# Performance work log

Hardware: AMD Instinct MI355X
Metric: run time of the kernel (lower is better)

## Reference

```python
import jax, jax.numpy as jnp
import numpy as np

N_HEADS = 32
N_KV_HEADS = 8
HEAD_DIM = 128
ROPE_BASE = 10000.0
NEG_INF = -1e9


def rope(x, base=ROPE_BASE, offset=0):
    # x: [B, H, L, d]; 'traditional' RoPE with the module's rotation formula.
    d = x.shape[-1]
    t = jnp.arange(x.shape[2], dtype=jnp.float32) + offset
    freqs = base ** (-jnp.arange(0, d, 2, dtype=jnp.float32) / d)  # [d/2]
    ang = t[:, None] * freqs[None, :]                              # [L, d/2]
    cos, sin = jnp.cos(ang), jnp.sin(ang)
    x1, x2 = x[..., 0::2], x[..., 1::2]
    out = jnp.stack([x1 * cos + x2 * sin, x1 * sin - x2 * cos], axis=-1)
    return out.reshape(x.shape)


def setup_inputs() -> dict:
    key = jax.random.key(0)
    ks = jax.random.split(key, 5)
    B, L, D = 2, 2048, 4096
    x = jax.random.normal(ks[0], (B, L, D), dtype=jnp.float32)
    wq = jax.random.normal(ks[1], (D, N_HEADS * HEAD_DIM), dtype=jnp.float32) * 0.02
    wk = jax.random.normal(ks[2], (D, N_KV_HEADS * HEAD_DIM), dtype=jnp.float32) * 0.02
    wv = jax.random.normal(ks[3], (D, N_KV_HEADS * HEAD_DIM), dtype=jnp.float32) * 0.02
    wo = jax.random.normal(ks[4], (N_HEADS * HEAD_DIM, D), dtype=jnp.float32) * 0.02
    # causal additive mask [L, L]
    mask = jnp.where(jnp.tril(jnp.ones((L, L), dtype=bool)), 0.0, NEG_INF).astype(jnp.float32)
    return {"x": x, "mask": mask, "wq": wq, "wk": wk, "wv": wv, "wo": wo}


def reference(x, mask, wq, wk, wv, wo):
    B, L, D = x.shape
    scale = HEAD_DIM ** -0.5
    q = (x @ wq).reshape(B, L, N_HEADS, HEAD_DIM).transpose(0, 2, 1, 3)     # [B,H,L,d]
    k = (x @ wk).reshape(B, L, N_KV_HEADS, HEAD_DIM).transpose(0, 2, 1, 3)  # [B,Hk,L,d]
    v = (x @ wv).reshape(B, L, N_KV_HEADS, HEAD_DIM).transpose(0, 2, 1, 3)
    rep = N_HEADS // N_KV_HEADS
    k = jnp.repeat(k, rep, axis=1)  # [B,H,L,d]  (physical GQA repeat, as in source)
    v = jnp.repeat(v, rep, axis=1)
    q = rope(q)
    k = rope(k)
    scores = jnp.einsum("bhqd,bhkd->bhqk", q * scale, k) + mask  # [B,H,L,L]
    probs = jax.nn.softmax(scores.astype(jnp.float32), axis=-1).astype(scores.dtype)
    out = jnp.einsum("bhqk,bhkd->bhqd", probs, v)
    out = out.transpose(0, 2, 1, 3).reshape(B, L, N_HEADS * HEAD_DIM)
    return out @ wo, (k, v)
```

## Files before the change

kernel.cpp:

```cpp
#include <hip/hip_runtime.h>

typedef unsigned short u16;
typedef unsigned int u32;
typedef float f32x4 __attribute__((ext_vector_type(4)));
typedef u32 u32x2 __attribute__((ext_vector_type(2)));
typedef __bf16 bf16x8 __attribute__((ext_vector_type(8)));

#define DEV __device__ __forceinline__

DEV u16 f2b(float f) {
    union { float f; u32 u; } v; v.f = f;
    u32 r = v.u + 0x7fffu + ((v.u >> 16) & 1u);
    return (u16)(r >> 16);
}
DEV float b2f(u16 b) {
    union { u32 u; float f; } v; v.u = ((u32)b) << 16;
    return v.f;
}

DEV void gload16(const void* g, void* l) {
    __builtin_amdgcn_global_load_lds((const __attribute__((address_space(1))) void*)g,
                                     (__attribute__((address_space(3))) void*)l, 16, 0, 0);
}

DEV f32x4 mfma16(bf16x8 a, bf16x8 b, f32x4 c) {
    return __builtin_amdgcn_mfma_f32_16x16x32_bf16(a, b, c, 0, 0, 0);
}

__global__ __launch_bounds__(256) void convx_kernel(const float* __restrict__ in,
                                                    u16* __restrict__ out) {
    size_t i = ((size_t)blockIdx.x * 256 + threadIdx.x) * 4;
    float4 v = *(const float4*)(in + i);
    ushort4 o; o.x = f2b(v.x); o.y = f2b(v.y); o.z = f2b(v.z); o.w = f2b(v.w);
    *(ushort4*)(out + i) = o;
}

__global__ __launch_bounds__(256) void tconv_kernel(const float* __restrict__ in,
                                                    u16* __restrict__ out, int K, int N) {
    __shared__ float tile[64][65];
    int t = threadIdx.x;
    int n0 = blockIdx.x * 64, k0 = blockIdx.y * 64;
    int r = t >> 4, c4 = (t & 15) * 4;
#pragma unroll
    for (int i = 0; i < 4; ++i) {
        float4 v = *(const float4*)(in + (size_t)(k0 + i * 16 + r) * N + n0 + c4);
        tile[i * 16 + r][c4 + 0] = v.x; tile[i * 16 + r][c4 + 1] = v.y;
        tile[i * 16 + r][c4 + 2] = v.z; tile[i * 16 + r][c4 + 3] = v.w;
    }
    __syncthreads();
#pragma unroll
    for (int i = 0; i < 4; ++i) {
        int nn = i * 16 + r;
        ushort4 o;
        o.x = f2b(tile[c4 + 0][nn]); o.y = f2b(tile[c4 + 1][nn]);
        o.z = f2b(tile[c4 + 2][nn]); o.w = f2b(tile[c4 + 3][nn]);
        *(ushort4*)(out + (size_t)(n0 + nn) * K + k0 + c4) = o;
    }
}

__global__ __launch_bounds__(512, 1) void gemm192_kernel(const u16* __restrict__ A,
                                                         const u16* __restrict__ Bt,
                                                         u16* __restrict__ Cb,
                                                         int N, int K, int gy) {
    __shared__ __align__(16) u16 Asb[2][2][128 * 64];
    __shared__ __align__(16) u16 Bsb[2][192 * 64];
    int t = threadIdx.x;
    int lane = t & 63, w = t >> 6;
    int wrM = w >> 2, wcN = w & 3;
    int lr = lane & 15, hi = lane >> 4;
    int wg = blockIdx.x;
    int swz = (wg & 7) * ((int)gridDim.x >> 3) + (wg >> 3);
    int bx = swz / gy, by = swz % gy;
    int m0 = by * 256, n0 = bx * 192;
    int nk = K >> 6;

    auto stageA = [&](int X) {
        const u16* src = A + (size_t)m0 * K + X * 64;
        char* dst = (char*)&Asb[X & 1][0][0];
#pragma unroll
        for (int it = 0; it < 4; ++it) {
            int c = it * 512 + t;
            int row = c >> 3;
            int col8 = ((c & 7) ^ (row & 7)) << 3;
            gload16(src + (size_t)row * K + col8, dst + (it * 512 + (t & ~63)) * 16);
        }
    };
    auto stageB = [&](int X) {
        const u16* src = Bt + (size_t)n0 * K + X * 64;
        char* dst = (char*)&Bsb[X & 1][0];
#pragma unroll
        for (int it = 0; it < 3; ++it) {
            int c = it * 512 + t;
            int row = c >> 3;
            int col8 = ((c & 7) ^ (row & 7)) << 3;
            gload16(src + (size_t)row * K + col8, dst + (it * 512 + (t & ~63)) * 16);
        }
    };

    stageA(0); stageB(0); stageA(1); stageB(1);
    asm volatile("s_waitcnt vmcnt(7)" ::: "memory");
    __builtin_amdgcn_s_barrier();

    f32x4 acc[8][3] = {};
    for (int kt = 0; kt < nk; ++kt) {
        __builtin_amdgcn_sched_barrier(0);
        int p = kt & 1;
        const char* Ah = (const char*)&Asb[p][wrM][0];
        const char* Bh = (const char*)&Bsb[p][0];
        bool s1 = (kt + 1 < nk), s2 = (kt + 2 < nk);
        bf16x8 a[8][2], bb[2][2], bc[2];

#pragma unroll
        for (int mf = 0; mf < 4; ++mf)
#pragma unroll
            for (int ks = 0; ks < 2; ++ks) {
                int row = mf * 16 + lr;
                a[mf][ks] = *(const bf16x8*)(Ah + ((row * 128 + ks * 64 + hi * 16) ^ ((row & 7) << 4)));
            }
#pragma unroll
        for (int nf = 0; nf < 2; ++nf)
#pragma unroll
            for (int ks = 0; ks < 2; ++ks) {
                int row = wcN * 48 + nf * 16 + lr;
                bb[nf][ks] = *(const bf16x8*)(Bh + ((row * 128 + ks * 64 + hi * 16) ^ ((row & 7) << 4)));
            }
        __builtin_amdgcn_s_barrier();
        __builtin_amdgcn_s_setprio(1);
#pragma unroll
        for (int mf = 0; mf < 4; ++mf)
#pragma unroll
            for (int nf = 0; nf < 2; ++nf)
#pragma unroll
                for (int ks = 0; ks < 2; ++ks)
                    acc[mf][nf] = mfma16(a[mf][ks], bb[nf][ks], acc[mf][nf]);
        __builtin_amdgcn_s_setprio(0);
        __builtin_amdgcn_s_barrier();

#pragma unroll
        for (int mf = 4; mf < 8; ++mf)
#pragma unroll
            for (int ks = 0; ks < 2; ++ks) {
                int row = mf * 16 + lr;
                a[mf][ks] = *(const bf16x8*)(Ah + ((row * 128 + ks * 64 + hi * 16) ^ ((row & 7) << 4)));
            }
        __builtin_amdgcn_s_barrier();
        __builtin_amdgcn_s_setprio(1);
#pragma unroll
        for (int mf = 4; mf < 8; ++mf)
#pragma unroll
            for (int nf = 0; nf < 2; ++nf)
#pragma unroll
                for (int ks = 0; ks < 2; ++ks)
                    acc[mf][nf] = mfma16(a[mf][ks], bb[nf][ks], acc[mf][nf]);
        __builtin_amdgcn_s_setprio(0);
        __builtin_amdgcn_s_barrier();

#pragma unroll
        for (int ks = 0; ks < 2; ++ks) {
            int row = wcN * 48 + 32 + lr;
            bc[ks] = *(const bf16x8*)(Bh + ((row * 128 + ks * 64 + hi * 16) ^ ((row & 7) << 4)));
        }
        if (s2) stageA(kt + 2);
        __builtin_amdgcn_s_barrier();
        __builtin_amdgcn_s_setprio(1);
#pragma unroll
        for (int mf = 4; mf < 8; ++mf)
#pragma unroll
            for (int ks = 0; ks < 2; ++ks)
                acc[mf][2] = mfma16(a[mf][ks], bc[ks], acc[mf][2]);
        __builtin_amdgcn_s_setprio(0);
        __builtin_amdgcn_s_barrier();

        if (s2) stageB(kt + 2);
        __builtin_amdgcn_s_barrier();
        __builtin_amdgcn_s_setprio(1);
#pragma unroll
        for (int mf = 0; mf < 4; ++mf)
#pragma unroll
            for (int ks = 0; ks < 2; ++ks)
                acc[mf][2] = mfma16(a[mf][ks], bc[ks], acc[mf][2]);
        __builtin_amdgcn_s_setprio(0);
        if (s1) {
            if (s2) asm volatile("s_waitcnt vmcnt(7)" ::: "memory");
            else    asm volatile("s_waitcnt vmcnt(0)" ::: "memory");
        }
        __builtin_amdgcn_s_barrier();
    }

#pragma unroll
    for (int mf = 0; mf < 8; ++mf)
#pragma unroll
        for (int nf = 0; nf < 3; ++nf)
#pragma unroll
            for (int r = 0; r < 4; ++r) {
                int m = m0 + wrM * 128 + mf * 16 + hi * 4 + r;
                int n = n0 + wcN * 48 + nf * 16 + lr;
                Cb[(size_t)m * N + n] = f2b(acc[mf][nf][r]);
            }
}

template <bool F32OUT>
__global__ __launch_bounds__(512, 1) void gemm256_kernel(const u16* __restrict__ A,
                                                         const u16* __restrict__ Bt,
                                                         u16* __restrict__ Cb,
                                                         float* __restrict__ Cf,
                                                         int M, int N, int K, int gy) {
    __shared__ __align__(16) u16 Asb[2][2][128 * 64];
    __shared__ __align__(16) u16 Bsb[2][2][128 * 64];
    (void)M;
    int t = threadIdx.x;
    int lane = t & 63, w = t >> 6;
    int wrM = w >> 2, wcN = w & 3;
    int lr = lane & 15, hi = lane >> 4;
    int wg = blockIdx.x;
    int swz = (wg & 7) * ((int)gridDim.x >> 3) + (wg >> 3);
    int bx = swz / gy, by = swz % gy;
    int m0 = by * 256, n0 = bx * 256;
    int nk = K >> 6;

    auto stageA = [&](int X, int h) {
        const u16* src = A + (size_t)(m0 + h * 128) * K + X * 64;
        char* dst = (char*)&Asb[X & 1][h][0];
#pragma unroll
        for (int it = 0; it < 2; ++it) {
            int c = it * 512 + t;
            int row = c >> 3;
            int col8 = ((c & 7) ^ (row & 7)) << 3;
            gload16(src + (size_t)row * K + col8, dst + (it * 512 + (t & ~63)) * 16);
        }
    };
    auto stageB = [&](int X, int h) {
        const u16* src = Bt + (size_t)(n0 + h * 128) * K + X * 64;
        char* dst = (char*)&Bsb[X & 1][h][0];
#pragma unroll
        for (int it = 0; it < 2; ++it) {
            int c = it * 512 + t;
            int row = c >> 3;
            int col8 = ((c & 7) ^ (row & 7)) << 3;
            gload16(src + (size_t)row * K + col8, dst + (it * 512 + (t & ~63)) * 16);
        }
    };

    stageA(0, 0); stageA(0, 1); stageB(0, 0); stageB(0, 1);
    stageA(1, 0); stageA(1, 1); stageB(1, 0);
    asm volatile("s_waitcnt vmcnt(6)" ::: "memory");
    __builtin_amdgcn_s_barrier();

    f32x4 acc[8][4] = {};
    for (int kt = 0; kt < nk; ++kt) {
        __builtin_amdgcn_sched_barrier(0);
        int p = kt & 1;
        const char* Ah = (const char*)&Asb[p][wrM][0];
        const char* Bh = (const char*)&Bsb[p][wcN >> 1][0];
        bool s1 = (kt + 1 < nk), s2 = (kt + 2 < nk);
        bf16x8 a[8][2], bb[2][2];

#pragma unroll
        for (int mf = 0; mf < 4; ++mf)
#pragma unroll
            for (int ks = 0; ks < 2; ++ks) {
                int row = mf * 16 + lr;
                a[mf][ks] = *(const bf16x8*)(Ah + ((row * 128 + ks * 64 + hi * 16) ^ ((row & 7) << 4)));
            }
#pragma unroll
        for (int nf = 0; nf < 2; ++nf)
#pragma unroll
            for (int ks = 0; ks < 2; ++ks) {
                int row = (wcN & 1) * 64 + nf * 16 + lr;
                bb[nf][ks] = *(const bf16x8*)(Bh + ((row * 128 + ks * 64 + hi * 16) ^ ((row & 7) << 4)));
            }
        if (s1) stageB(kt + 1, 1);
        __builtin_amdgcn_s_barrier();
        __builtin_amdgcn_s_setprio(1);
#pragma unroll
        for (int mf = 0; mf < 4; ++mf)
#pragma unroll
            for (int nf = 0; nf < 2; ++nf)
#pragma unroll
                for (int ks = 0; ks < 2; ++ks)
                    acc[mf][nf] = mfma16(a[mf][ks], bb[nf][ks], acc[mf][nf]);
        __builtin_amdgcn_s_setprio(0);
        __builtin_amdgcn_s_barrier();

#pragma unroll
        for (int mf = 4; mf < 8; ++mf)
#pragma unroll
            for (int ks = 0; ks < 2; ++ks) {
                int row = mf * 16 + lr;
                a[mf][ks] = *(const bf16x8*)(Ah + ((row * 128 + ks * 64 + hi * 16) ^ ((row & 7) << 4)));
            }
        __builtin_amdgcn_s_barrier();
        __builtin_amdgcn_s_setprio(1);
#pragma unroll
        for (int mf = 4; mf < 8; ++mf)
#pragma unroll
            for (int nf = 0; nf < 2; ++nf)
#pragma unroll
                for (int ks = 0; ks < 2; ++ks)
                    acc[mf][nf] = mfma16(a[mf][ks], bb[nf][ks], acc[mf][nf]);
        __builtin_amdgcn_s_setprio(0);
        __builtin_amdgcn_s_barrier();

#pragma unroll
        for (int nf = 0; nf < 2; ++nf)
#pragma unroll
            for (int ks = 0; ks < 2; ++ks) {
                int row = (wcN & 1) * 64 + (nf + 2) * 16 + lr;
                bb[nf][ks] = *(const bf16x8*)(Bh + ((row * 128 + ks * 64 + hi * 16) ^ ((row & 7) << 4)));
            }
        if (s2) { stageA(kt + 2, 0); stageA(kt + 2, 1); }
        __builtin_amdgcn_s_barrier();
        __builtin_amdgcn_s_setprio(1);
#pragma unroll
        for (int mf = 4; mf < 8; ++mf)
#pragma unroll
            for (int nf = 0; nf < 2; ++nf)
#pragma unroll
                for (int ks = 0; ks < 2; ++ks)
                    acc[mf][nf + 2] = mfma16(a[mf][ks], bb[nf][ks], acc[mf][nf + 2]);
        __builtin_amdgcn_s_setprio(0);
        __builtin_amdgcn_s_barrier();

        if (s2) stageB(kt + 2, 0);
        __builtin_amdgcn_s_barrier();
        __builtin_amdgcn_s_setprio(1);
#pragma unroll
        for (int mf = 0; mf < 4; ++mf)
#pragma unroll
            for (int nf = 0; nf < 2; ++nf)
#pragma unroll
                for (int ks = 0; ks < 2; ++ks)
                    acc[mf][nf + 2] = mfma16(a[mf][ks], bb[nf][ks], acc[mf][nf + 2]);
        __builtin_amdgcn_s_setprio(0);
        if (s1) {
            if (s2) asm volatile("s_waitcnt vmcnt(6)" ::: "memory");
            else    asm volatile("s_waitcnt vmcnt(0)" ::: "memory");
        }
        __builtin_amdgcn_s_barrier();
    }

#pragma unroll
    for (int mf = 0; mf < 8; ++mf)
#pragma unroll
        for (int nf = 0; nf < 4; ++nf)
#pragma unroll
            for (int r = 0; r < 4; ++r) {
                int m = m0 + wrM * 128 + mf * 16 + hi * 4 + r;
                int n = n0 + wcN * 64 + nf * 16 + lr;
                if (F32OUT) Cf[(size_t)m * N + n] = acc[mf][nf][r];
                else        Cb[(size_t)m * N + n] = f2b(acc[mf][nf][r]);
            }
}

__global__ __launch_bounds__(256) void rope_kernel(u16* __restrict__ qkv,
                                                   float* __restrict__ outk) {
    int row = blockIdx.y;
    int p = blockIdx.x * 256 + threadIdx.x;
    int b = row >> 11, l = row & 2047;
    float freq = exp2f((float)(p & 63) * -0.2076205059304601f);
    float sv, cv; sincosf((float)l * freq, &sv, &cv);
    if (p < 2048) {
        int h = p >> 6, i = p & 63;
        size_t idx = (size_t)row * 6144 + h * 128 + 2 * i;
        u32 pr = *(const u32*)(qkv + idx);
        float x1 = b2f((u16)(pr & 0xffff)), x2 = b2f((u16)(pr >> 16));
        float o1 = x1 * cv + x2 * sv, o2 = x1 * sv - x2 * cv;
        *(u32*)(qkv + idx) = (u32)f2b(o1) | ((u32)f2b(o2) << 16);
    } else {
        int kvh = (p >> 6) - 32, i = p & 63;
        size_t idx = (size_t)row * 6144 + 4096 + kvh * 128 + 2 * i;
        u32 pr = *(const u32*)(qkv + idx);
        float x1 = b2f((u16)(pr & 0xffff)), x2 = b2f((u16)(pr >> 16));
        float o1 = x1 * cv + x2 * sv, o2 = x1 * sv - x2 * cv;
        *(u32*)(qkv + idx) = (u32)f2b(o1) | ((u32)f2b(o2) << 16);
#pragma unroll
        for (int r = 0; r < 4; ++r) {
            float2 o; o.x = o1; o.y = o2;
            *(float2*)(outk + ((size_t)((b * 32 + kvh * 4 + r) * 2048) + l) * 128 + 2 * i) = o;
        }
    }
}

__global__ __launch_bounds__(256) void vtrans_kernel(const u16* __restrict__ qkv,
                                                     u16* __restrict__ vt,
                                                     float* __restrict__ outv) {
    __shared__ u16 tile[64][65];
    int t = threadIdx.x;
    int l0 = blockIdx.x * 64, d0 = blockIdx.y * 64;
    int z = blockIdx.z, b = z >> 3, kvh = z & 7;
    int r = t >> 4, c4 = (t & 15) * 4;
#pragma unroll
    for (int i = 0; i < 4; ++i) {
        int l = l0 + i * 16 + r;
        ushort4 v = *(const ushort4*)(qkv + (size_t)(b * 2048 + l) * 6144 + 5120 + kvh * 128 + d0 + c4);
        tile[i * 16 + r][c4 + 0] = v.x; tile[i * 16 + r][c4 + 1] = v.y;
        tile[i * 16 + r][c4 + 2] = v.z; tile[i * 16 + r][c4 + 3] = v.w;
        float4 f; f.x = b2f(v.x); f.y = b2f(v.y); f.z = b2f(v.z); f.w = b2f(v.w);
#pragma unroll
        for (int rr = 0; rr < 4; ++rr)
            *(float4*)(outv + ((size_t)((b * 32 + kvh * 4 + rr) * 2048) + l) * 128 + d0 + c4) = f;
    }
    __syncthreads();
#pragma unroll
    for (int i = 0; i < 4; ++i) {
        int dn = i * 16 + r;
        ushort4 o;
        o.x = tile[c4 + 0][dn]; o.y = tile[c4 + 1][dn];
        o.z = tile[c4 + 2][dn]; o.w = tile[c4 + 3][dn];
        *(ushort4*)(vt + (size_t)((b * 8 + kvh) * 128 + d0 + dn) * 2048 + l0 + c4) = o;
    }
}

__global__ __launch_bounds__(256) void attn_kernel(const u16* __restrict__ qkv,
                                                   const u16* __restrict__ vt,
                                                   u16* __restrict__ ab) {
    __shared__ __align__(16) u16 Kbuf[2][64 * 128];
    __shared__ __align__(16) u16 Vbuf[2][128 * 64];
    __shared__ __align__(16) u16 Ps[4][16 * 64];
    int t = threadIdx.x, lane = t & 63, w = t >> 6;
    int lr = lane & 15, hi = lane >> 4;
    int h = blockIdx.y, b = blockIdx.z, kvh = h >> 2;

    const u16* kbase = qkv + (size_t)(b * 2048) * 6144 + 4096 + kvh * 128;
    const u16* vtbase = vt + (size_t)((b * 8 + kvh) * 128) * 2048;

    auto stageKV = [&](int k0, int buf) {
#pragma unroll
        for (int i = 0; i < 4; ++i) {
            int c = i * 256 + t;
            int row = c >> 4;
            int col8 = ((c & 15) ^ (row & 7)) << 3;
            gload16(kbase + (size_t)(k0 + row) * 6144 + col8,
                    (char*)Kbuf[buf] + (i * 256 + (t & ~63)) * 16);
        }
#pragma unroll
        for (int i = 0; i < 4; ++i) {
            int c = i * 256 + t;
            int row = c >> 3;
            int col8 = ((c & 7) ^ (row & 7)) << 3;
            gload16(vtbase + (size_t)row * 2048 + k0 + col8,
                    (char*)Vbuf[buf] + (i * 256 + (t & ~63)) * 16);
        }
    };

    auto process = [&](int qblk) {
        int q0 = qblk * 64;
        int qr = w * 16 + lr;
        bf16x8 qf[4];
#pragma unroll
        for (int kki = 0; kki < 4; ++kki)
            qf[kki] = *(const bf16x8*)(qkv + (size_t)(b * 2048 + q0 + qr) * 6144 + h * 128 +
                                       kki * 32 + 8 * hi);
        f32x4 acc[8] = {};
        float mrun = -1e30f, lrun = 0.f;

        int nt = qblk + 1;
        stageKV(0, 0);
        __syncthreads();
        int cur = 0;
        for (int kt = 0; kt < nt; ++kt) {
            if (kt + 1 < nt) stageKV((kt + 1) * 64, cur ^ 1);
            __builtin_amdgcn_sched_barrier(0);

            const u16* Ks = Kbuf[cur];
            const u16* Vs = Vbuf[cur];
            f32x4 s[4] = {};
            __builtin_amdgcn_s_setprio(1);
#pragma unroll
            for (int kki = 0; kki < 4; ++kki) {
                bf16x8 kf[4];
#pragma unroll
                for (int fc = 0; fc < 4; ++fc) {
                    int kvr = fc * 16 + lr;
                    int byt = (kvr * 256 + (kki * 32 + 8 * hi) * 2) ^ ((kvr & 7) << 4);
                    kf[fc] = *(const bf16x8*)((const char*)Ks + byt);
                }
#pragma unroll
                for (int fc = 0; fc < 4; ++fc) s[fc] = mfma16(kf[fc], qf[kki], s[fc]);
            }
            __builtin_amdgcn_s_setprio(0);
            const float SC = 0.08838834764831845f;
            int diag = (kt == nt - 1);
#pragma unroll
            for (int fc = 0; fc < 4; ++fc)
#pragma unroll
                for (int r = 0; r < 4; ++r) {
                    float v = s[fc][r] * SC;
                    if (diag && (fc * 16 + hi * 4 + r) > qr) v = -1e30f;
                    s[fc][r] = v;
                }
            float pm = s[0][0];
#pragma unroll
            for (int fc = 0; fc < 4; ++fc)
#pragma unroll
                for (int r = 0; r < 4; ++r) pm = fmaxf(pm, s[fc][r]);
            pm = fmaxf(pm, __shfl_xor(pm, 16));
            pm = fmaxf(pm, __shfl_xor(pm, 32));
            float mn = fmaxf(mrun, pm);
            float fr = __expf(mrun - mn);
            mrun = mn;
            float ls = 0.f;
#pragma unroll
            for (int fc = 0; fc < 4; ++fc)
#pragma unroll
                for (int r = 0; r < 4; ++r) {
                    float e = __expf(s[fc][r] - mn);
                    s[fc][r] = e;
                    ls += e;
                }
            ls += __shfl_xor(ls, 16);
            ls += __shfl_xor(ls, 32);
            lrun = lrun * fr + ls;
#pragma unroll
            for (int dhf = 0; dhf < 8; ++dhf)
#pragma unroll
                for (int r = 0; r < 4; ++r) acc[dhf][r] *= fr;
            u16* Pw = Ps[w];
#pragma unroll
            for (int fc = 0; fc < 4; ++fc) {
                u32x2 pk;
                pk.x = (u32)f2b(s[fc][0]) | ((u32)f2b(s[fc][1]) << 16);
                pk.y = (u32)f2b(s[fc][2]) | ((u32)f2b(s[fc][3]) << 16);
                int byt = (lr * 128 + fc * 32 + hi * 8) ^ ((lr & 7) << 4);
                *(u32x2*)((char*)Pw + byt) = pk;
            }
            asm volatile("s_waitcnt lgkmcnt(0)" ::: "memory");
            __builtin_amdgcn_s_setprio(1);
#pragma unroll
            for (int kk2 = 0; kk2 < 2; ++kk2) {
                int bytp = (lr * 128 + kk2 * 64 + hi * 16) ^ ((lr & 7) << 4);
                bf16x8 pf = *(const bf16x8*)((const char*)Pw + bytp);
#pragma unroll
                for (int dhf = 0; dhf < 8; ++dhf) {
                    int dh = dhf * 16 + lr;
                    int bytv = (dh * 128 + (kk2 * 32 + 8 * hi) * 2) ^ ((dh & 7) << 4);
                    bf16x8 vf = *(const bf16x8*)((const char*)Vs + bytv);
                    acc[dhf] = mfma16(vf, pf, acc[dhf]);
                }
            }
            __builtin_amdgcn_s_setprio(0);
            __syncthreads();
            cur ^= 1;
        }
        float inv = 1.0f / lrun;
        int qrow = q0 + qr;
#pragma unroll
        for (int dhf = 0; dhf < 8; ++dhf) {
            ushort4 o;
            o.x = f2b(acc[dhf][0] * inv); o.y = f2b(acc[dhf][1] * inv);
            o.z = f2b(acc[dhf][2] * inv); o.w = f2b(acc[dhf][3] * inv);
            *(ushort4*)(ab + (size_t)(b * 2048 + qrow) * 4096 + h * 128 + dhf * 16 + hi * 4) = o;
        }
    };

    process(31 - blockIdx.x);
    __syncthreads();
    process(blockIdx.x);
}

extern "C" void kernel_launch(void* const* d_in, const int* in_sizes, int n_in,
                              void* d_out, int out_size, void* d_ws, size_t ws_size,
                              hipStream_t stream) {
    (void)in_sizes; (void)n_in; (void)out_size; (void)ws_size;
    const float* x  = (const float*)d_in[0];
    const float* wq = (const float*)d_in[2];
    const float* wk = (const float*)d_in[3];
    const float* wv = (const float*)d_in[4];
    const float* wo = (const float*)d_in[5];

    char* ws = (char*)d_ws;
    u16* xb  = (u16*)(ws + 0);
    u16* fBt = (u16*)(ws + 33554432);
    u16* qkv = (u16*)(ws + 83886080);
    u16* vt  = (u16*)(ws + 134217728);
    u16* ab  = xb;
    u16* wob = fBt;

    float* out0 = (float*)d_out;
    float* outk = out0 + 16777216;
    float* outv = out0 + 33554432;

    convx_kernel<<<16384, 256, 0, stream>>>(x, xb);
    tconv_kernel<<<dim3(64, 64), 256, 0, stream>>>(wq, fBt, 4096, 4096);
    tconv_kernel<<<dim3(16, 64), 256, 0, stream>>>(wk, fBt + (size_t)4096 * 4096, 4096, 1024);
    tconv_kernel<<<dim3(16, 64), 256, 0, stream>>>(wv, fBt + (size_t)5120 * 4096, 4096, 1024);

    gemm192_kernel<<<512, 512, 0, stream>>>(xb, fBt, qkv, 6144, 4096, 16);

    tconv_kernel<<<dim3(64, 64), 256, 0, stream>>>(wo, wob, 4096, 4096);

    rope_kernel<<<dim3(10, 4096), 256, 0, stream>>>(qkv, outk);
    vtrans_kernel<<<dim3(32, 2, 16), 256, 0, stream>>>(qkv, vt, outv);

    attn_kernel<<<dim3(16, 32, 2), 256, 0, stream>>>(qkv, vt, ab);

    gemm256_kernel<true><<<256, 512, 0, stream>>>(ab, wob, nullptr, out0, 4096, 4096, 4096, 16);
}
```

Measured before the change: 616.5 us.

## Enlarge attention query tile to 128 rows per block for K/V reuse

Each attention block now handles 128 query rows (32 per wave, two 16-row halves) instead of 64, so every staged K/V tile feeds twice as many MFMAs and K/V global traffic per query is halved. The grid shrinks from 16 to 8 blocks in x, and the causal pairing becomes process(15-x) and process(x). The change adds per-wave register pressure (two accumulator sets and two softmax states) and doubles the P scratch buffer in shared memory. The launch bounds now request 2 blocks per CU, and the grid has half as many blocks.

```diff
diff --git a/kernel.cpp b/kernel.cpp
--- a/kernel.cpp
+++ b/kernel.cpp
@@ -411,12 +411,12 @@
     }
 }
 
-__global__ __launch_bounds__(256) void attn_kernel(const u16* __restrict__ qkv,
-                                                   const u16* __restrict__ vt,
-                                                   u16* __restrict__ ab) {
+__global__ __launch_bounds__(256, 2) void attn_kernel(const u16* __restrict__ qkv,
+                                                      const u16* __restrict__ vt,
+                                                      u16* __restrict__ ab) {
     __shared__ __align__(16) u16 Kbuf[2][64 * 128];
     __shared__ __align__(16) u16 Vbuf[2][128 * 64];
-    __shared__ __align__(16) u16 Ps[4][16 * 64];
+    __shared__ __align__(16) u16 Ps[4][32 * 64];
     int t = threadIdx.x, lane = t & 63, w = t >> 6;
     int lr = lane & 15, hi = lane >> 4;
     int h = blockIdx.y, b = blockIdx.z, kvh = h >> 2;
@@ -444,17 +444,19 @@
     };
 
     auto process = [&](int qblk) {
-        int q0 = qblk * 64;
-        int qr = w * 16 + lr;
-        bf16x8 qf[4];
-#pragma unroll
-        for (int kki = 0; kki < 4; ++kki)
-            qf[kki] = *(const bf16x8*)(qkv + (size_t)(b * 2048 + q0 + qr) * 6144 + h * 128 +
-                                       kki * 32 + 8 * hi);
-        f32x4 acc[8] = {};
-        float mrun = -1e30f, lrun = 0.f;
-
-        int nt = qblk + 1;
+        int q0 = qblk * 128;
+        bf16x8 qf[2][4];
+#pragma unroll
+        for (int half = 0; half < 2; ++half)
+#pragma unroll
+            for (int kki = 0; kki < 4; ++kki)
+                qf[half][kki] = *(const bf16x8*)(qkv +
+                    (size_t)(b * 2048 + q0 + w * 32 + half * 16 + lr) * 6144 + h * 128 +
+                    kki * 32 + 8 * hi);
+        f32x4 acc[2][8] = {};
+        float mrun[2] = {-1e30f, -1e30f}, lrun[2] = {0.f, 0.f};
+
+        int nt = 2 * (qblk + 1);
         stageKV(0, 0);
         __syncthreads();
         int cur = 0;
@@ -464,7 +466,7 @@
 
             const u16* Ks = Kbuf[cur];
             const u16* Vs = Vbuf[cur];
-            f32x4 s[4] = {};
+            f32x4 s[2][4] = {};
             __builtin_amdgcn_s_setprio(1);
 #pragma unroll
             for (int kki = 0; kki < 4; ++kki) {
@@ -476,84 +478,97 @@
                     kf[fc] = *(const bf16x8*)((const char*)Ks + byt);
                 }
 #pragma unroll
-                for (int fc = 0; fc < 4; ++fc) s[fc] = mfma16(kf[fc], qf[kki], s[fc]);
+                for (int fc = 0; fc < 4; ++fc) {
+                    s[0][fc] = mfma16(kf[fc], qf[0][kki], s[0][fc]);
+                    s[1][fc] = mfma16(kf[fc], qf[1][kki], s[1][fc]);
+                }
             }
             __builtin_amdgcn_s_setprio(0);
             const float SC = 0.08838834764831845f;
-            int diag = (kt == nt - 1);
-#pragma unroll
-            for (int fc = 0; fc < 4; ++fc)
-#pragma unroll
-                for (int r = 0; r < 4; ++r) {
-                    float v = s[fc][r] * SC;
-                    if (diag && (fc * 16 + hi * 4 + r) > qr) v = -1e30f;
-                    s[fc][r] = v;
+            int domask = (kt >= nt - 2);
+            u16* Pw = Ps[w];
+#pragma unroll
+            for (int half = 0; half < 2; ++half) {
+                int qabs = q0 + w * 32 + half * 16 + lr;
+#pragma unroll
+                for (int fc = 0; fc < 4; ++fc)
+#pragma unroll
+                    for (int r = 0; r < 4; ++r) {
+                        float v = s[half][fc][r] * SC;
+                        if (domask && (kt * 64 + fc * 16 + hi * 4 + r) > qabs) v = -1e30f;
+                        s[half][fc][r] = v;
+                    }
+                float pm = s[half][0][0];
+#pragma unroll
+                for (int fc = 0; fc < 4; ++fc)
+#pragma unroll
+                    for (int r = 0; r < 4; ++r) pm = fmaxf(pm, s[half][fc][r]);
+                pm = fmaxf(pm, __shfl_xor(pm, 16));
+                pm = fmaxf(pm, __shfl_xor(pm, 32));
+                float mn = fmaxf(mrun[half], pm);
+                float fr = __expf(mrun[half] - mn);
+                mrun[half] = mn;
+                float ls = 0.f;
+#pragma unroll
+                for (int fc = 0; fc < 4; ++fc)
+#pragma unroll
+                    for (int r = 0; r < 4; ++r) {
+                        float e = __expf(s[half][fc][r] - mn);
+                        s[half][fc][r] = e;
+                        ls += e;
+                    }
+                ls += __shfl_xor(ls, 16);
+                ls += __shfl_xor(ls, 32);
+                lrun[half] = lrun[half] * fr + ls;
+#pragma unroll
+                for (int dhf = 0; dhf < 8; ++dhf)
+#pragma unroll
+                    for (int r = 0; r < 4; ++r) acc[half][dhf][r] *= fr;
+#pragma unroll
+                for (int fc = 0; fc < 4; ++fc) {
+                    u32x2 pk;
+                    pk.x = (u32)f2b(s[half][fc][0]) | ((u32)f2b(s[half][fc][1]) << 16);
+                    pk.y = (u32)f2b(s[half][fc][2]) | ((u32)f2b(s[half][fc][3]) << 16);
+                    int byt = (half * 2048 + lr * 128 + fc * 32 + hi * 8) ^ ((lr & 7) << 4);
+                    *(u32x2*)((char*)Pw + byt) = pk;
                 }
-            float pm = s[0][0];
-#pragma unroll
-            for (int fc = 0; fc < 4; ++fc)
-#pragma unroll
-                for (int r = 0; r < 4; ++r) pm = fmaxf(pm, s[fc][r]);
-            pm = fmaxf(pm, __shfl_xor(pm, 16));
-            pm = fmaxf(pm, __shfl_xor(pm, 32));
-            float mn = fmaxf(mrun, pm);
-            float fr = __expf(mrun - mn);
-            mrun = mn;
-            float ls = 0.f;
-#pragma unroll
-            for (int fc = 0; fc < 4; ++fc)
-#pragma unroll
-                for (int r = 0; r < 4; ++r) {
-                    float e = __expf(s[fc][r] - mn);
-                    s[fc][r] = e;
-                    ls += e;
-                }
-            ls += __shfl_xor(ls, 16);
-            ls += __shfl_xor(ls, 32);
-            lrun = lrun * fr + ls;
-#pragma unroll
-            for (int dhf = 0; dhf < 8; ++dhf)
-#pragma unroll
-                for (int r = 0; r < 4; ++r) acc[dhf][r] *= fr;
-            u16* Pw = Ps[w];
-#pragma unroll
-            for (int fc = 0; fc < 4; ++fc) {
-                u32x2 pk;
-                pk.x = (u32)f2b(s[fc][0]) | ((u32)f2b(s[fc][1]) << 16);
-                pk.y = (u32)f2b(s[fc][2]) | ((u32)f2b(s[fc][3]) << 16);
-                int byt = (lr * 128 + fc * 32 + hi * 8) ^ ((lr & 7) << 4);
-                *(u32x2*)((char*)Pw + byt) = pk;
             }
             asm volatile("s_waitcnt lgkmcnt(0)" ::: "memory");
             __builtin_amdgcn_s_setprio(1);
 #pragma unroll
             for (int kk2 = 0; kk2 < 2; ++kk2) {
-                int bytp = (lr * 128 + kk2 * 64 + hi * 16) ^ ((lr & 7) << 4);
-                bf16x8 pf = *(const bf16x8*)((const char*)Pw + bytp);
+                bf16x8 pf0 = *(const bf16x8*)((const char*)Pw +
+                    ((lr * 128 + kk2 * 64 + hi * 16) ^ ((lr & 7) << 4)));
+                bf16x8 pf1 = *(const bf16x8*)((const char*)Pw +
+                    ((2048 + lr * 128 + kk2 * 64 + hi * 16) ^ ((lr & 7) << 4)));
 #pragma unroll
                 for (int dhf = 0; dhf < 8; ++dhf) {
                     int dh = dhf * 16 + lr;
                     int bytv = (dh * 128 + (kk2 * 32 + 8 * hi) * 2) ^ ((dh & 7) << 4);
                     bf16x8 vf = *(const bf16x8*)((const char*)Vs + bytv);
-                    acc[dhf] = mfma16(vf, pf, acc[dhf]);
+                    acc[0][dhf] = mfma16(vf, pf0, acc[0][dhf]);
+                    acc[1][dhf] = mfma16(vf, pf1, acc[1][dhf]);
                 }
             }
             __builtin_amdgcn_s_setprio(0);
             __syncthreads();
             cur ^= 1;
         }
-        float inv = 1.0f / lrun;
-        int qrow = q0 + qr;
-#pragma unroll
-        for (int dhf = 0; dhf < 8; ++dhf) {
-            ushort4 o;
-            o.x = f2b(acc[dhf][0] * inv); o.y = f2b(acc[dhf][1] * inv);
-            o.z = f2b(acc[dhf][2] * inv); o.w = f2b(acc[dhf][3] * inv);
-            *(ushort4*)(ab + (size_t)(b * 2048 + qrow) * 4096 + h * 128 + dhf * 16 + hi * 4) = o;
+#pragma unroll
+        for (int half = 0; half < 2; ++half) {
+            float inv = 1.0f / lrun[half];
+            int qrow = q0 + w * 32 + half * 16 + lr;
+#pragma unroll
+            for (int dhf = 0; dhf < 8; ++dhf) {
+                ushort4 o;
+                o.x = f2b(acc[half][dhf][0] * inv); o.y = f2b(acc[half][dhf][1] * inv);
+                o.z = f2b(acc[half][dhf][2] * inv); o.w = f2b(acc[half][dhf][3] * inv);
+                *(ushort4*)(ab + (size_t)(b * 2048 + qrow) * 4096 + h * 128 + dhf * 16 + hi * 4) = o;
+            }
         }
     };
 
-    process(31 - blockIdx.x);
+    process(15 - blockIdx.x);
     __syncthreads();
     process(blockIdx.x);
 }
@@ -592,7 +607,7 @@
     rope_kernel<<<dim3(10, 4096), 256, 0, stream>>>(qkv, outk);
     vtrans_kernel<<<dim3(32, 2, 16), 256, 0, stream>>>(qkv, vt, outv);
 
-    attn_kernel<<<dim3(16, 32, 2), 256, 0, stream>>>(qkv, vt, ab);
+    attn_kernel<<<dim3(8, 32, 2), 256, 0, stream>>>(qkv, vt, ab);
 
     gemm256_kernel<true><<<256, 512, 0, stream>>>(ab, wob, nullptr, out0, 4096, 4096, 4096, 16);
 }
```

New measurement: 591.5 us. 1.04x faster.
